# Optimization experiments

Measured on AMD Instinct MI355X. Metric: run time of the kernel, lower is better.

The kernel has to match this reference:

```python
import jax, jax.numpy as jnp
import numpy as np

IN_FEATURES = 128
OUT_FEATURES = 128


def setup_inputs() -> dict:
    key = jax.random.key(0)
    k1, k2, k3 = jax.random.split(key, 3)
    h_i = jax.random.normal(k1, (IN_FEATURES,), dtype=jnp.float32)
    h_j = jax.random.normal(k2, (200000, OUT_FEATURES), dtype=jnp.float32)
    a = jax.random.normal(k3, (IN_FEATURES + OUT_FEATURES, 1), dtype=jnp.float32)
    return {"h_i": h_i, "h_j": h_j, "a": a}


def reference(h_i, h_j, a):
    # e_n = dot(concat(h_i, h_j[n]), a) = h_i . a[:in] + h_j[n] . a[in:]
    a_i = a[:IN_FEATURES, 0]   # [in]
    a_j = a[IN_FEATURES:, 0]   # [out]
    logits = jnp.dot(h_i, a_i) + h_j @ a_j        # [N]
    attention = jax.nn.softmax(logits, axis=0)    # [N]
    # dropout is identity in eval mode (training=False)
    h_prime = attention @ h_j                     # [out]
    return jax.nn.elu(h_prime)                    # concat=True -> ELU
```

## Files before the change

### kernel.cpp

```cpp
#include <hip/hip_runtime.h>
#include <math.h>

#define COLS 128
#define NB   1024
#define BIAS2 57.70780163555853f
#define LOG2E 1.4426950408889634f

__global__ __launch_bounds__(256) void gat_pass1(
    const float* __restrict__ hj, const float* __restrict__ a,
    float* __restrict__ pacc, float* __restrict__ pl,
    int nrows, int nunits) {
  const int t    = threadIdx.x;
  const int sub  = t & 15;
  const int uq   = t >> 4;
  const int unit = blockIdx.x * 16 + uq;
  const int stride = nunits;

  const float4 aj0 = ((const float4*)(a + COLS))[sub];
  const float4 aj1 = ((const float4*)(a + COLS + 64))[sub];

  float4 acc0 = make_float4(0.f, 0.f, 0.f, 0.f);
  float4 acc1 = make_float4(0.f, 0.f, 0.f, 0.f);
  float l = 0.f;

  int r = unit;
  for (; r + 3 * stride < nrows; r += 4 * stride) {
    const float* b0 = hj + (size_t)r * COLS;
    const float* b1 = hj + (size_t)(r + stride) * COLS;
    const float* b2 = hj + (size_t)(r + 2 * stride) * COLS;
    const float* b3 = hj + (size_t)(r + 3 * stride) * COLS;
    const float4 v0a = ((const float4*)b0)[sub], v0b = ((const float4*)(b0 + 64))[sub];
    const float4 v1a = ((const float4*)b1)[sub], v1b = ((const float4*)(b1 + 64))[sub];
    const float4 v2a = ((const float4*)b2)[sub], v2b = ((const float4*)(b2 + 64))[sub];
    const float4 v3a = ((const float4*)b3)[sub], v3b = ((const float4*)(b3 + 64))[sub];

    float p0 = v0a.x*aj0.x + v0a.y*aj0.y + v0a.z*aj0.z + v0a.w*aj0.w
             + v0b.x*aj1.x + v0b.y*aj1.y + v0b.z*aj1.z + v0b.w*aj1.w;
    float p1 = v1a.x*aj0.x + v1a.y*aj0.y + v1a.z*aj0.z + v1a.w*aj0.w
             + v1b.x*aj1.x + v1b.y*aj1.y + v1b.z*aj1.z + v1b.w*aj1.w;
    float p2 = v2a.x*aj0.x + v2a.y*aj0.y + v2a.z*aj0.z + v2a.w*aj0.w
             + v2b.x*aj1.x + v2b.y*aj1.y + v2b.z*aj1.z + v2b.w*aj1.w;
    float p3 = v3a.x*aj0.x + v3a.y*aj0.y + v3a.z*aj0.z + v3a.w*aj0.w
             + v3b.x*aj1.x + v3b.y*aj1.y + v3b.z*aj1.z + v3b.w*aj1.w;
    #pragma unroll
    for (int off = 1; off <= 8; off <<= 1) {
      p0 += __shfl_xor(p0, off);
      p1 += __shfl_xor(p1, off);
      p2 += __shfl_xor(p2, off);
      p3 += __shfl_xor(p3, off);
    }
    const float w0 = __builtin_amdgcn_exp2f(fmaf(p0, LOG2E, -BIAS2));
    const float w1 = __builtin_amdgcn_exp2f(fmaf(p1, LOG2E, -BIAS2));
    const float w2 = __builtin_amdgcn_exp2f(fmaf(p2, LOG2E, -BIAS2));
    const float w3 = __builtin_amdgcn_exp2f(fmaf(p3, LOG2E, -BIAS2));
    l += (w0 + w1) + (w2 + w3);
    acc0.x += w0*v0a.x + w1*v1a.x + w2*v2a.x + w3*v3a.x;
    acc0.y += w0*v0a.y + w1*v1a.y + w2*v2a.y + w3*v3a.y;
    acc0.z += w0*v0a.z + w1*v1a.z + w2*v2a.z + w3*v3a.z;
    acc0.w += w0*v0a.w + w1*v1a.w + w2*v2a.w + w3*v3a.w;
    acc1.x += w0*v0b.x + w1*v1b.x + w2*v2b.x + w3*v3b.x;
    acc1.y += w0*v0b.y + w1*v1b.y + w2*v2b.y + w3*v3b.y;
    acc1.z += w0*v0b.z + w1*v1b.z + w2*v2b.z + w3*v3b.z;
    acc1.w += w0*v0b.w + w1*v1b.w + w2*v2b.w + w3*v3b.w;
  }
  for (; r < nrows; r += stride) {
    const float* b0 = hj + (size_t)r * COLS;
    const float4 va = ((const float4*)b0)[sub], vb = ((const float4*)(b0 + 64))[sub];
    float p = va.x*aj0.x + va.y*aj0.y + va.z*aj0.z + va.w*aj0.w
            + vb.x*aj1.x + vb.y*aj1.y + vb.z*aj1.z + vb.w*aj1.w;
    #pragma unroll
    for (int off = 1; off <= 8; off <<= 1) p += __shfl_xor(p, off);
    const float w = __builtin_amdgcn_exp2f(fmaf(p, LOG2E, -BIAS2));
    l += w;
    acc0.x += w*va.x; acc0.y += w*va.y; acc0.z += w*va.z; acc0.w += w*va.w;
    acc1.x += w*vb.x; acc1.y += w*vb.y; acc1.z += w*vb.z; acc1.w += w*vb.w;
  }

  __shared__ float sacc[16][COLS + 4];
  __shared__ float sl[16];
  *((float4*)&sacc[uq][sub * 4])      = acc0;
  *((float4*)&sacc[uq][64 + sub * 4]) = acc1;
  if (sub == 0) sl[uq] = l;
  __syncthreads();

  if (t < COLS) {
    float s = 0.f;
    #pragma unroll
    for (int u = 0; u < 16; u++) s += sacc[u][t];
    pacc[(size_t)blockIdx.x * COLS + t] = s;
  } else if (t == COLS) {
    float lb = 0.f;
    #pragma unroll
    for (int u = 0; u < 16; u++) lb += sl[u];
    pl[blockIdx.x] = lb;
  }
}

__global__ __launch_bounds__(256) void gat_pass2(
    const float* __restrict__ pacc, const float* __restrict__ pl,
    float* __restrict__ out, int nblocks) {
  const int col = blockIdx.x;
  const int t   = threadIdx.x;
  const int lane = t & 63;
  const int wave = t >> 6;
  __shared__ float sz[4], sc[4];

  float zs = 0.f, cs = 0.f;
  for (int b = t; b < nblocks; b += 256) {
    zs += pl[b];
    cs += pacc[(size_t)b * COLS + col];
  }
  #pragma unroll
  for (int off = 1; off < 64; off <<= 1) {
    zs += __shfl_xor(zs, off);
    cs += __shfl_xor(cs, off);
  }
  if (lane == 0) { sz[wave] = zs; sc[wave] = cs; }
  __syncthreads();

  if (t == 0) {
    const float Z = sz[0] + sz[1] + sz[2] + sz[3];
    const float C = sc[0] + sc[1] + sc[2] + sc[3];
    const float h = C / Z;
    out[col] = h > 0.f ? h : expm1f(h);
  }
}

extern "C" void kernel_launch(void* const* d_in, const int* in_sizes, int n_in,
                              void* d_out, int out_size, void* d_ws, size_t ws_size,
                              hipStream_t stream) {
  const float* hj = (const float*)d_in[1];
  const float* a  = (const float*)d_in[2];
  float* out = (float*)d_out;

  const int nrows = in_sizes[1] / COLS;

  int nblocks = NB;
  const size_t per_block = (COLS + 1) * sizeof(float);
  if (ws_size < (size_t)nblocks * per_block) {
    nblocks = (int)(ws_size / per_block);
    if (nblocks > 64) nblocks &= ~63;
    if (nblocks < 1) nblocks = 1;
  }
  const int nunits = nblocks * 16;

  float* pacc = (float*)d_ws;
  float* pl   = pacc + (size_t)nblocks * COLS;

  gat_pass1<<<nblocks, 256, 0, stream>>>(hj, a, pacc, pl, nrows, nunits);
  gat_pass2<<<COLS, 256, 0, stream>>>(pacc, pl, out, nblocks);
}
```

Before: 154.5 us.

## Stage contiguous row chunks through double-buffered LDS with direct global-to-LDS loads

Each block now owns a contiguous chunk of 196 rows instead of striding across the whole matrix. It streams 32-row tiles into a double-buffered shared-memory area using global_load_lds DMA, prefetching the next tile while it computes the current one. A rotated column index (cs) spreads shared-memory reads across banks. The aim is better DRAM locality and more loads in flight. In exchange it adds two block barriers per tile, and it hardcodes the grid to 1024 blocks without the old workspace-size check, so other row counts are only covered up to 1024×196 rows.

Measured after the change: 157.5 us. About the same (+1.9%).

```diff
diff --git a/kernel.cpp b/kernel.cpp
--- a/kernel.cpp
+++ b/kernel.cpp
@@ -1,97 +1,98 @@
 #include <hip/hip_runtime.h>
 #include <math.h>
 
-#define COLS 128
-#define NB   1024
-#define BIAS2 57.70780163555853f
-#define LOG2E 1.4426950408889634f
+#define COLS   128
+#define NBLK   1024
+#define CHUNK  196
+#define TROWS  32
+#define TILEF  (TROWS * COLS)
+#define LOG2E  1.4426950408889634f
+#define BIAS2  57.70780163555853f
+
+typedef __attribute__((address_space(1))) void as1_void;
+typedef __attribute__((address_space(3))) void as3_void;
+
+__device__ __forceinline__ void dma16(const float* g, float* l) {
+  __builtin_amdgcn_global_load_lds((as1_void*)g, (as3_void*)l, 16, 0, 0);
+}
 
 __global__ __launch_bounds__(256) void gat_pass1(
     const float* __restrict__ hj, const float* __restrict__ a,
-    float* __restrict__ pacc, float* __restrict__ pl,
-    int nrows, int nunits) {
+    float* __restrict__ pacc, float* __restrict__ pl, int nrows) {
+  __shared__ float smem[2 * TILEF];
+  __shared__ float sl2[16];
+
   const int t    = threadIdx.x;
+  const int wave = t >> 6;
+  const int lane = t & 63;
+  const int q    = t >> 4;
   const int sub  = t & 15;
-  const int uq   = t >> 4;
-  const int unit = blockIdx.x * 16 + uq;
-  const int stride = nunits;
+  const int cs   = (sub + ((q & 3) << 2)) & 15;
 
-  const float4 aj0 = ((const float4*)(a + COLS))[sub];
-  const float4 aj1 = ((const float4*)(a + COLS + 64))[sub];
+  const float4 ajA = *(const float4*)&a[COLS + cs * 4];
+  const float4 ajB = *(const float4*)&a[COLS + 64 + cs * 4];
+
+  const int base  = blockIdx.x * CHUNK;
+  const int cnt   = (nrows - base < CHUNK) ? (nrows - base) : CHUNK;
+  const int nt    = (cnt > 0) ? ((cnt + TROWS - 1) / TROWS) : 0;
+  const int limit = base + (cnt > 0 ? cnt : 0);
 
   float4 acc0 = make_float4(0.f, 0.f, 0.f, 0.f);
   float4 acc1 = make_float4(0.f, 0.f, 0.f, 0.f);
   float l = 0.f;
 
-  int r = unit;
-  for (; r + 3 * stride < nrows; r += 4 * stride) {
-    const float* b0 = hj + (size_t)r * COLS;
-    const float* b1 = hj + (size_t)(r + stride) * COLS;
-    const float* b2 = hj + (size_t)(r + 2 * stride) * COLS;
-    const float* b3 = hj + (size_t)(r + 3 * stride) * COLS;
-    const float4 v0a = ((const float4*)b0)[sub], v0b = ((const float4*)(b0 + 64))[sub];
-    const float4 v1a = ((const float4*)b1)[sub], v1b = ((const float4*)(b1 + 64))[sub];
-    const float4 v2a = ((const float4*)b2)[sub], v2b = ((const float4*)(b2 + 64))[sub];
-    const float4 v3a = ((const float4*)b3)[sub], v3b = ((const float4*)(b3 + 64))[sub];
+  auto stage = [&](int ti) {
+    const int boff = (ti & 1) * TILEF;
+    #pragma unroll
+    for (int k = 0; k < 4; ++k) {
+      const int ch   = wave * 4 + k;
+      const int trow = 2 * ch + (lane >> 5);
+      const int arow = base + ti * TROWS + trow;
+      if (arow < nrows)
+        dma16(hj + (size_t)arow * COLS + (lane & 31) * 4, &smem[boff + ch * 256]);
+    }
+  };
 
-    float p0 = v0a.x*aj0.x + v0a.y*aj0.y + v0a.z*aj0.z + v0a.w*aj0.w
-             + v0b.x*aj1.x + v0b.y*aj1.y + v0b.z*aj1.z + v0b.w*aj1.w;
-    float p1 = v1a.x*aj0.x + v1a.y*aj0.y + v1a.z*aj0.z + v1a.w*aj0.w
-             + v1b.x*aj1.x + v1b.y*aj1.y + v1b.z*aj1.z + v1b.w*aj1.w;
-    float p2 = v2a.x*aj0.x + v2a.y*aj0.y + v2a.z*aj0.z + v2a.w*aj0.w
-             + v2b.x*aj1.x + v2b.y*aj1.y + v2b.z*aj1.z + v2b.w*aj1.w;
-    float p3 = v3a.x*aj0.x + v3a.y*aj0.y + v3a.z*aj0.z + v3a.w*aj0.w
-             + v3b.x*aj1.x + v3b.y*aj1.y + v3b.z*aj1.z + v3b.w*aj1.w;
+  if (nt > 0) stage(0);
+  for (int i = 0; i < nt; ++i) {
+    if (i + 1 < nt) stage(i + 1);
+    __syncthreads();
+    const int boff = (i & 1) * TILEF;
+    const int tb   = base + i * TROWS;
     #pragma unroll
-    for (int off = 1; off <= 8; off <<= 1) {
-      p0 += __shfl_xor(p0, off);
-      p1 += __shfl_xor(p1, off);
-      p2 += __shfl_xor(p2, off);
-      p3 += __shfl_xor(p3, off);
+    for (int rr = 0; rr < 2; ++rr) {
+      const int trow = q + 16 * rr;
+      const int arow = tb + trow;
+      if (arow < limit) {
+        const float4 vA = *(const float4*)&smem[boff + trow * COLS + cs * 4];
+        const float4 vB = *(const float4*)&smem[boff + trow * COLS + 64 + cs * 4];
+        float p = vA.x * ajA.x + vA.y * ajA.y + vA.z * ajA.z + vA.w * ajA.w
+                + vB.x * ajB.x + vB.y * ajB.y + vB.z * ajB.z + vB.w * ajB.w;
+        #pragma unroll
+        for (int off = 1; off <= 8; off <<= 1) p += __shfl_xor(p, off);
+        const float w = __builtin_amdgcn_exp2f(fmaf(p, LOG2E, -BIAS2));
+        l += w;
+        acc0.x += w * vA.x; acc0.y += w * vA.y; acc0.z += w * vA.z; acc0.w += w * vA.w;
+        acc1.x += w * vB.x; acc1.y += w * vB.y; acc1.z += w * vB.z; acc1.w += w * vB.w;
+      }
     }
-    const float w0 = __builtin_amdgcn_exp2f(fmaf(p0, LOG2E, -BIAS2));
-    const float w1 = __builtin_amdgcn_exp2f(fmaf(p1, LOG2E, -BIAS2));
-    const float w2 = __builtin_amdgcn_exp2f(fmaf(p2, LOG2E, -BIAS2));
-    const float w3 = __builtin_amdgcn_exp2f(fmaf(p3, LOG2E, -BIAS2));
-    l += (w0 + w1) + (w2 + w3);
-    acc0.x += w0*v0a.x + w1*v1a.x + w2*v2a.x + w3*v3a.x;
-    acc0.y += w0*v0a.y + w1*v1a.y + w2*v2a.y + w3*v3a.y;
-    acc0.z += w0*v0a.z + w1*v1a.z + w2*v2a.z + w3*v3a.z;
-    acc0.w += w0*v0a.w + w1*v1a.w + w2*v2a.w + w3*v3a.w;
-    acc1.x += w0*v0b.x + w1*v1b.x + w2*v2b.x + w3*v3b.x;
-    acc1.y += w0*v0b.y + w1*v1b.y + w2*v2b.y + w3*v3b.y;
-    acc1.z += w0*v0b.z + w1*v1b.z + w2*v2b.z + w3*v3b.z;
-    acc1.w += w0*v0b.w + w1*v1b.w + w2*v2b.w + w3*v3b.w;
-  }
-  for (; r < nrows; r += stride) {
-    const float* b0 = hj + (size_t)r * COLS;
-    const float4 va = ((const float4*)b0)[sub], vb = ((const float4*)(b0 + 64))[sub];
-    float p = va.x*aj0.x + va.y*aj0.y + va.z*aj0.z + va.w*aj0.w
-            + vb.x*aj1.x + vb.y*aj1.y + vb.z*aj1.z + vb.w*aj1.w;
-    #pragma unroll
-    for (int off = 1; off <= 8; off <<= 1) p += __shfl_xor(p, off);
-    const float w = __builtin_amdgcn_exp2f(fmaf(p, LOG2E, -BIAS2));
-    l += w;
-    acc0.x += w*va.x; acc0.y += w*va.y; acc0.z += w*va.z; acc0.w += w*va.w;
-    acc1.x += w*vb.x; acc1.y += w*vb.y; acc1.z += w*vb.z; acc1.w += w*vb.w;
+    __syncthreads();
   }
 
-  __shared__ float sacc[16][COLS + 4];
-  __shared__ float sl[16];
-  *((float4*)&sacc[uq][sub * 4])      = acc0;
-  *((float4*)&sacc[uq][64 + sub * 4]) = acc1;
-  if (sub == 0) sl[uq] = l;
+  *(float4*)&smem[q * 132 + cs * 4]      = acc0;
+  *(float4*)&smem[q * 132 + 64 + cs * 4] = acc1;
+  if (sub == 0) sl2[q] = l;
   __syncthreads();
 
   if (t < COLS) {
     float s = 0.f;
     #pragma unroll
-    for (int u = 0; u < 16; u++) s += sacc[u][t];
+    for (int u = 0; u < 16; ++u) s += smem[u * 132 + t];
     pacc[(size_t)blockIdx.x * COLS + t] = s;
   } else if (t == COLS) {
     float lb = 0.f;
     #pragma unroll
-    for (int u = 0; u < 16; u++) lb += sl[u];
+    for (int u = 0; u < 16; ++u) lb += sl2[u];
     pl[blockIdx.x] = lb;
   }
 }
@@ -99,8 +100,8 @@
 __global__ __launch_bounds__(256) void gat_pass2(
     const float* __restrict__ pacc, const float* __restrict__ pl,
     float* __restrict__ out, int nblocks) {
-  const int col = blockIdx.x;
-  const int t   = threadIdx.x;
+  const int col  = blockIdx.x;
+  const int t    = threadIdx.x;
   const int lane = t & 63;
   const int wave = t >> 6;
   __shared__ float sz[4], sc[4];
@@ -135,18 +136,9 @@
 
   const int nrows = in_sizes[1] / COLS;
 
-  int nblocks = NB;
-  const size_t per_block = (COLS + 1) * sizeof(float);
-  if (ws_size < (size_t)nblocks * per_block) {
-    nblocks = (int)(ws_size / per_block);
-    if (nblocks > 64) nblocks &= ~63;
-    if (nblocks < 1) nblocks = 1;
-  }
-  const int nunits = nblocks * 16;
+  float* pacc = (float*)d_ws;
+  float* pl   = pacc + (size_t)NBLK * COLS;
 
-  float* pacc = (float*)d_ws;
-  float* pl   = pacc + (size_t)nblocks * COLS;
-
-  gat_pass1<<<nblocks, 256, 0, stream>>>(hj, a, pacc, pl, nrows, nunits);
-  gat_pass2<<<COLS, 256, 0, stream>>>(pacc, pl, out, nblocks);
+  gat_pass1<<<NBLK, 256, 0, stream>>>(hj, a, pacc, pl, nrows);
+  gat_pass2<<<COLS, 256, 0, stream>>>(pacc, pl, out, NBLK);
 }
```
